# Kernel optimization log

Measured on AMD Instinct MI355X. Metric: run time of the kernel, lower is better.

## Reference

```python
import jax, jax.numpy as jnp
import numpy as np

DIM_MODEL = 512
DIM_HEAD = 64


def setup_inputs() -> dict:
    key = jax.random.key(0)
    ks = jax.random.split(key, 7)
    B, S = 4, 4096
    scale = 1.0 / np.sqrt(DIM_MODEL)
    x = jax.random.normal(ks[0], (B, S, DIM_MODEL), dtype=jnp.float32)
    # nn.Linear weights: stored as [out, in] in torch; we use [in, out] for x @ W
    Wq = jax.random.uniform(ks[1], (DIM_MODEL, DIM_HEAD), jnp.float32, -scale, scale)
    Wk = jax.random.uniform(ks[2], (DIM_MODEL, DIM_HEAD), jnp.float32, -scale, scale)
    Wv = jax.random.uniform(ks[3], (DIM_MODEL, DIM_HEAD), jnp.float32, -scale, scale)
    bq = jax.random.uniform(ks[4], (DIM_HEAD,), jnp.float32, -scale, scale)
    bk = jax.random.uniform(ks[5], (DIM_HEAD,), jnp.float32, -scale, scale)
    bv = jax.random.uniform(ks[6], (DIM_HEAD,), jnp.float32, -scale, scale)
    return {"x": x, "Wq": Wq, "bq": bq, "Wk": Wk, "bk": bk, "Wv": Wv, "bv": bv}


def reference(x, Wq, bq, Wk, bk, Wv, bv):
    # [q,k,v] = z @ U_qkv
    q = x @ Wq + bq  # [B, S, Dh]
    k = x @ Wk + bk
    v = x @ Wv + bv
    dot_scale = jnp.sqrt(jnp.asarray(DIM_HEAD, dtype=x.dtype))
    scores = jnp.einsum("bsd,btd->bst", q, k) / dot_scale  # [B, S, S]
    attn = jax.nn.softmax(scores, axis=-1)
    return jnp.einsum("bst,btd->bsd", attn, v)  # [B, S, Dh]
```

## Files before the change

kernel.cpp:

```cpp
#include <hip/hip_runtime.h>
#include <hip/hip_bf16.h>

typedef short short8 __attribute__((ext_vector_type(8)));
typedef float f32x4 __attribute__((ext_vector_type(4)));

#define MFMA16(a,b,c) __builtin_amdgcn_mfma_f32_16x16x32_bf16((a),(b),(c),0,0,0)

#define NROWS 16384
#define LOG2E 1.44269504088896340736f

#define OFF_Q  0u
#define OFF_K  (2u<<20)
#define OFF_V  (4u<<20)
#define OFF_W  (6u<<20)
#define OFF_O  ((6u<<20) + (1u<<18))

__device__ __forceinline__ unsigned short f2bf(float f){
    union { float f; unsigned u; } v; v.f = f;
    unsigned r = v.u + 0x7FFFu + ((v.u >> 16) & 1u);
    return (unsigned short)(r >> 16);
}
__device__ __forceinline__ unsigned pk2(float a, float b){
    union { __hip_bfloat162 h; unsigned u; } c;
    c.h = __float22bfloat162_rn(make_float2(a, b));
    return c.u;
}

union Frag {
    short8 s;
    unsigned short u[8];
    uint2 d2[2];
    uint4 q4;
};

__global__ __launch_bounds__(256) void wprep_kernel(
    const float* __restrict__ Wq, const float* __restrict__ Wk,
    const float* __restrict__ Wv, unsigned short* __restrict__ wfrag)
{
    int idx = blockIdx.x * 256 + threadIdx.x;
    int lane = idx & 63;
    int rest = idx >> 6;
    int kk = rest & 15;
    int nt = (rest >> 4) & 3;
    int w  = rest >> 6;
    const float* W = (w == 0) ? Wq : (w == 1) ? Wk : Wv;
    float scl = (w == 0) ? (0.125f * LOG2E) : 1.0f;
    int n = 16 * nt + (lane & 15);
    int g = lane >> 4;
    Frag o;
#pragma unroll
    for (int e = 0; e < 8; ++e) {
        int k = 32 * kk + 16 * (e >> 2) + 4 * g + (e & 3);
        o.u[e] = f2bf(W[k * 64 + n] * scl);
    }
    *(uint4*)(wfrag + (size_t)idx * 8) = o.q4;
}

#define LDW(WD, KK) do { \
    _Pragma("unroll") \
    for (int nt_ = 0; nt_ < 4; ++nt_) \
        WD[nt_].q4 = wf[((size_t)(nt_ * 16 + (KK))) * 64 + lane]; \
    } while (0)

#define DOK(WC, KK) do { \
    _Pragma("unroll") \
    for (int M_ = 0; M_ < 2; ++M_) { \
        Frag xf_; \
        const unsigned short* xr_ = &xs[M_ * 16 + l15][32 * (KK) + 4 * g]; \
        xf_.d2[0] = *(const uint2*)xr_; \
        xf_.d2[1] = *(const uint2*)(xr_ + 16); \
        if (w == 2) { \
            _Pragma("unroll") \
            for (int nt_ = 0; nt_ < 4; ++nt_) acc[M_][nt_] = MFMA16(xf_.s, WC[nt_].s, acc[M_][nt_]); \
        } else { \
            _Pragma("unroll") \
            for (int nt_ = 0; nt_ < 4; ++nt_) acc[M_][nt_] = MFMA16(WC[nt_].s, xf_.s, acc[M_][nt_]); \
        } \
    } } while (0)

__global__ __launch_bounds__(192) void qkv_kernel(
    const float* __restrict__ x,
    const float* __restrict__ bq, const float* __restrict__ bk,
    const float* __restrict__ bv,
    const unsigned short* __restrict__ wfrag,
    unsigned short* __restrict__ qfrag,
    unsigned short* __restrict__ kfrag,
    unsigned short* __restrict__ vfrag)
{
    __shared__ unsigned short xs[32][520];
    const int tid = threadIdx.x;
    const int lane = tid & 63;
    const int w = tid >> 6;
    const int l15 = lane & 15, g = lane >> 4;
    const int rg32 = blockIdx.x;
    const float* xbase = x + (size_t)rg32 * 32 * 512;

    for (int i = tid; i < 4096; i += 192) {
        float4 v = *(const float4*)(xbase + i * 4);
        int r_ = i >> 7;
        int c_ = (i & 127) * 4;
        *(uint2*)&xs[r_][c_] = make_uint2(pk2(v.x, v.y), pk2(v.z, v.w));
    }
    __syncthreads();

    f32x4 acc[2][4];
#pragma unroll
    for (int M = 0; M < 2; ++M)
#pragma unroll
        for (int nt = 0; nt < 4; ++nt) acc[M][nt] = (f32x4){0.f,0.f,0.f,0.f};

    const uint4* wf = (const uint4*)wfrag + (size_t)w * 4096;

    Frag wA[4], wB[4];
    LDW(wA, 0);
#pragma unroll
    for (int kp = 0; kp < 8; ++kp) {
        LDW(wB, 2 * kp + 1);
        __builtin_amdgcn_sched_barrier(0);
        DOK(wA, 2 * kp);
        if (2 * kp + 2 < 16) LDW(wA, 2 * kp + 2);
        __builtin_amdgcn_sched_barrier(0);
        DOK(wB, 2 * kp + 1);
    }

#pragma unroll
    for (int M = 0; M < 2; ++M) {
        const int rg  = rg32 * 2 + M;
        const int b   = rg >> 8;
        const int rgb = rg & 255;
        const int tc  = rgb >> 2;
        const int c   = rgb & 3;

        if (w == 0) {
#pragma unroll
            for (int nt = 0; nt < 4; ++nt) {
                float4 bb = *(const float4*)(bq + 16 * nt + 4 * g);
                const float bs = 0.125f * LOG2E;
                float q0 = acc[M][nt][0] + bb.x * bs;
                float q1 = acc[M][nt][1] + bb.y * bs;
                float q2 = acc[M][nt][2] + bb.z * bs;
                float q3 = acc[M][nt][3] + bb.w * bs;
                int ks = nt >> 1, h = nt & 1;
                size_t qoff = ((size_t)(rg * 2 + ks) * 64 + lane) * 8 + h * 4;
                *(uint2*)(qfrag + qoff) = make_uint2(pk2(q0, q1), pk2(q2, q3));
            }
        } else if (w == 1) {
#pragma unroll
            for (int nt = 0; nt < 4; ++nt) {
                float4 bb = *(const float4*)(bk + 16 * nt + 4 * g);
                float k0 = acc[M][nt][0] + bb.x;
                float k1 = acc[M][nt][1] + bb.y;
                float k2 = acc[M][nt][2] + bb.z;
                float k3 = acc[M][nt][3] + bb.w;
                int ks = nt >> 1, h = nt & 1;
                size_t kfi = ((size_t)((b * 64 + tc) * 4 + c) * 2 + ks);
                size_t koff = (kfi * 64 + lane) * 8 + h * 4;
                *(uint2*)(kfrag + koff) = make_uint2(pk2(k0, k1), pk2(k2, k3));
            }
        } else {
            const int vks = c >> 1, vh = c & 1;
#pragma unroll
            for (int nt = 0; nt < 4; ++nt) {
                float bvv = bv[16 * nt + l15];
                float v0 = acc[M][nt][0] + bvv;
                float v1 = acc[M][nt][1] + bvv;
                float v2 = acc[M][nt][2] + bvv;
                float v3 = acc[M][nt][3] + bvv;
                size_t vfi = ((size_t)((b * 64 + tc) * 4 + nt) * 2 + vks);
                size_t voff = (vfi * 64 + lane) * 8 + vh * 4;
                *(uint2*)(vfrag + voff) = make_uint2(pk2(v0, v1), pk2(v2, v3));
            }
        }
    }
}

#define LOADK(KD, CH) do { \
    const uint4* p_ = kb0 + (size_t)(CH) * 512; \
    _Pragma("unroll") \
    for (int c_ = 0; c_ < 4; ++c_) { \
        KD[c_][0].q4 = p_[(c_ * 2 + 0) * 64]; \
        KD[c_][1].q4 = p_[(c_ * 2 + 1) * 64]; \
    } } while (0)

#define LOADV(VD, CH) do { \
    const uint4* p_ = vb0 + (size_t)(CH) * 512; \
    _Pragma("unroll") \
    for (int c_ = 0; c_ < 4; ++c_) { \
        VD[c_][0].q4 = p_[(c_ * 2 + 0) * 64]; \
        VD[c_][1].q4 = p_[(c_ * 2 + 1) * 64]; \
    } } while (0)

#define BODY(KC, KN, CH, CHN) do { \
    Frag vC[4][2]; \
    LOADV(vC, CH); \
    LOADK(KN, CHN); \
    __builtin_amdgcn_sched_barrier(0); \
    _Pragma("unroll") \
    for (int M_ = 0; M_ < 4; ++M_) { \
        f32x4 sD[4]; \
        __builtin_amdgcn_s_setprio(1); \
        _Pragma("unroll") \
        for (int c_ = 0; c_ < 4; ++c_) { \
            f32x4 D = (f32x4){0.f,0.f,0.f,0.f}; \
            D = MFMA16(KC[c_][0].s, qf[M_][0].s, D); \
            D = MFMA16(KC[c_][1].s, qf[M_][1].s, D); \
            sD[c_] = D; \
        } \
        __builtin_amdgcn_s_setprio(0); \
        Frag pa0, pa1; \
        _Pragma("unroll") \
        for (int c_ = 0; c_ < 4; ++c_) { \
            float p0 = __builtin_exp2f(sD[c_][0]); \
            float p1 = __builtin_exp2f(sD[c_][1]); \
            float p2 = __builtin_exp2f(sD[c_][2]); \
            float p3 = __builtin_exp2f(sD[c_][3]); \
            uint2 pk_ = make_uint2(pk2(p0, p1), pk2(p2, p3)); \
            if (c_ < 2) pa0.d2[c_ & 1] = pk_; else pa1.d2[c_ & 1] = pk_; \
        } \
        __builtin_amdgcn_s_setprio(1); \
        lacc[M_] = MFMA16(pa0.s, ones_.s, lacc[M_]); \
        lacc[M_] = MFMA16(pa1.s, ones_.s, lacc[M_]); \
        _Pragma("unroll") \
        for (int dc_ = 0; dc_ < 4; ++dc_) { \
            acc[M_][dc_] = MFMA16(pa0.s, vC[dc_][0].s, acc[M_][dc_]); \
            acc[M_][dc_] = MFMA16(pa1.s, vC[dc_][1].s, acc[M_][dc_]); \
        } \
        __builtin_amdgcn_s_setprio(0); \
    } } while (0)

__global__ __launch_bounds__(256, 2) void attn_kernel(
    const unsigned short* __restrict__ qfrag,
    const unsigned short* __restrict__ kfrag,
    const unsigned short* __restrict__ vfrag,
    uint2* __restrict__ OpartU, float* __restrict__ lml,
    int CPS, int SBITS)
{
    const int tid = threadIdx.x;
    const int lane = tid & 63;
    const int w = tid >> 6;
    const int l15 = lane & 15, g = lane >> 4;
    const int split  = blockIdx.x & ((1 << SBITS) - 1);
    const int qblock = blockIdx.x >> SBITS;
    const int gw = qblock * 4 + w;
    const int b = gw >> 6;
    const int tcg0 = b * 64 + split * CPS;

    const uint4* qf4 = (const uint4*)qfrag;
    const uint4* kb0 = (const uint4*)kfrag + (size_t)tcg0 * 512 + lane;
    const uint4* vb0 = (const uint4*)vfrag + (size_t)tcg0 * 512 + lane;

    Frag qf[4][2];
#pragma unroll
    for (int M = 0; M < 4; ++M)
#pragma unroll
        for (int ks = 0; ks < 2; ++ks)
            qf[M][ks].q4 = qf4[((size_t)((gw * 4 + M) * 2 + ks)) * 64 + lane];

    Frag ones_;
    ones_.d2[0] = make_uint2(0x3F803F80u, 0x3F803F80u);
    ones_.d2[1] = make_uint2(0x3F803F80u, 0x3F803F80u);

    f32x4 acc[4][4], lacc[4];
#pragma unroll
    for (int M = 0; M < 4; ++M) {
        lacc[M] = (f32x4){0.f,0.f,0.f,0.f};
#pragma unroll
        for (int dc = 0; dc < 4; ++dc) acc[M][dc] = (f32x4){0.f,0.f,0.f,0.f};
    }

    Frag kA[4][2], kB[4][2];
    LOADK(kA, 0);

#pragma unroll 1
    for (int ch = 0; ch < CPS; ch += 2) {
        int c1 = (ch + 1 < CPS) ? (ch + 1) : ch;
        int c2 = (ch + 2 < CPS) ? (ch + 2) : ch;
        BODY(kA, kB, ch, c1);
        BODY(kB, kA, c1, c2);
    }

#pragma unroll
    for (int M = 0; M < 4; ++M) {
#pragma unroll
        for (int dc = 0; dc < 4; ++dc)
            OpartU[((size_t)(split * 256 + gw) * 16 + M * 4 + dc) * 64 + lane] =
                make_uint2(pk2(acc[M][dc][0], acc[M][dc][1]),
                           pk2(acc[M][dc][2], acc[M][dc][3]));
        if (l15 == 0)
            *(f32x4*)(lml + (size_t)(split * 256 + gw) * 64 + M * 16 + 4 * g) = lacc[M];
    }
}

__global__ __launch_bounds__(256) void merge_kernel(
    const uint2* __restrict__ OpartU, const float* __restrict__ lml,
    float* __restrict__ out, int S)
{
    int gid = blockIdx.x * 256 + threadIdx.x;
    int lane = gid & 63;
    int dc = (gid >> 6) & 3;
    int M  = (gid >> 8) & 3;
    int gw = gid >> 10;
    int l15 = lane & 15, g = lane >> 4;

    float o0 = 0.f, o1 = 0.f, o2 = 0.f, o3 = 0.f;
    float L0 = 0.f, L1 = 0.f, L2 = 0.f, L3 = 0.f;
    for (int s = 0; s < S; ++s) {
        uint2 pv = OpartU[((size_t)(s * 256 + gw) * 16 + M * 4 + dc) * 64 + lane];
        float4 lv = *(const float4*)(lml + (size_t)(s * 256 + gw) * 64 + M * 16 + 4 * g);
        o0 += __uint_as_float(pv.x << 16);
        o1 += __uint_as_float(pv.x & 0xFFFF0000u);
        o2 += __uint_as_float(pv.y << 16);
        o3 += __uint_as_float(pv.y & 0xFFFF0000u);
        L0 += lv.x; L1 += lv.y; L2 += lv.z; L3 += lv.w;
    }
    size_t row = (size_t)gw * 64 + M * 16 + 4 * g;
    int col = 16 * dc + l15;
    out[(row + 0) * 64 + col] = o0 / L0;
    out[(row + 1) * 64 + col] = o1 / L1;
    out[(row + 2) * 64 + col] = o2 / L2;
    out[(row + 3) * 64 + col] = o3 / L3;
}

extern "C" void kernel_launch(void* const* d_in, const int* in_sizes, int n_in,
                              void* d_out, int out_size, void* d_ws, size_t ws_size,
                              hipStream_t stream) {
    (void)in_sizes; (void)n_in; (void)out_size;
    const float* x  = (const float*)d_in[0];
    const float* Wq = (const float*)d_in[1];
    const float* bq = (const float*)d_in[2];
    const float* Wk = (const float*)d_in[3];
    const float* bk = (const float*)d_in[4];
    const float* Wv = (const float*)d_in[5];
    const float* bv = (const float*)d_in[6];
    float* out = (float*)d_out;

    char* ws = (char*)d_ws;
    unsigned short* qfrag = (unsigned short*)(ws + OFF_Q);
    unsigned short* kfrag = (unsigned short*)(ws + OFF_K);
    unsigned short* vfrag = (unsigned short*)(ws + OFF_V);
    unsigned short* wfrag = (unsigned short*)(ws + OFF_W);

    const size_t oneO = (size_t)256 * 16 * 64 * 8;
    const size_t oneL = (size_t)256 * 64 * 4;
    int S = 8, SBITS = 3;
    if (ws_size < (size_t)OFF_O + 8 * (oneO + oneL)) { S = 4; SBITS = 2; }
    if (ws_size < (size_t)OFF_O + 4 * (oneO + oneL)) { S = 2; SBITS = 1; }
    uint2* OpartU = (uint2*)(ws + OFF_O);
    float* lml    = (float*)(ws + OFF_O + (size_t)S * oneO);
    int CPS = 64 / S;

    hipLaunchKernelGGL(wprep_kernel, dim3(48), dim3(256), 0, stream,
                       Wq, Wk, Wv, wfrag);
    hipLaunchKernelGGL(qkv_kernel, dim3(512), dim3(192), 0, stream,
                       x, bq, bk, bv, wfrag, qfrag, kfrag, vfrag);
    hipLaunchKernelGGL(attn_kernel, dim3(64 * S), dim3(256), 0, stream,
                       qfrag, kfrag, vfrag, OpartU, lml, CPS, SBITS);
    hipLaunchKernelGGL(merge_kernel, dim3(1024), dim3(256), 0, stream,
                       OpartU, lml, out, S);
}
```

Measured before the change: 58.45 us.

## Fuse split-KV merge into attention kernel via last-block atomic counter

Removes the separate merge kernel launch: each attention block increments a per-query-block counter after writing its partial outputs, and the last split to finish reduces all splits and writes the final normalized output. Counters are zeroed in the weight-prep kernel. This saves a launch and its tail, but the merge now runs serially on one block per query block, using fewer threads than the old merge grid and adding threadfence and atomic overhead.

```diff
diff --git a/kernel.cpp b/kernel.cpp
--- a/kernel.cpp
+++ b/kernel.cpp
@@ -35,8 +35,10 @@
 
 __global__ __launch_bounds__(256) void wprep_kernel(
     const float* __restrict__ Wq, const float* __restrict__ Wk,
-    const float* __restrict__ Wv, unsigned short* __restrict__ wfrag)
+    const float* __restrict__ Wv, unsigned short* __restrict__ wfrag,
+    int* __restrict__ cnt)
 {
+    if (blockIdx.x == 0 && threadIdx.x < 256) cnt[threadIdx.x] = 0;
     int idx = blockIdx.x * 256 + threadIdx.x;
     int lane = idx & 63;
     int rest = idx >> 6;
@@ -233,8 +235,10 @@
     const unsigned short* __restrict__ kfrag,
     const unsigned short* __restrict__ vfrag,
     uint2* __restrict__ OpartU, float* __restrict__ lml,
+    int* __restrict__ cnt, float* __restrict__ out,
     int CPS, int SBITS)
 {
+    __shared__ int lastflag;
     const int tid = threadIdx.x;
     const int lane = tid & 63;
     const int w = tid >> 6;
@@ -289,36 +293,42 @@
         if (l15 == 0)
             *(f32x4*)(lml + (size_t)(split * 256 + gw) * 64 + M * 16 + 4 * g) = lacc[M];
     }
-}
-
-__global__ __launch_bounds__(256) void merge_kernel(
-    const uint2* __restrict__ OpartU, const float* __restrict__ lml,
-    float* __restrict__ out, int S)
-{
-    int gid = blockIdx.x * 256 + threadIdx.x;
-    int lane = gid & 63;
-    int dc = (gid >> 6) & 3;
-    int M  = (gid >> 8) & 3;
-    int gw = gid >> 10;
-    int l15 = lane & 15, g = lane >> 4;
-
-    float o0 = 0.f, o1 = 0.f, o2 = 0.f, o3 = 0.f;
-    float L0 = 0.f, L1 = 0.f, L2 = 0.f, L3 = 0.f;
-    for (int s = 0; s < S; ++s) {
-        uint2 pv = OpartU[((size_t)(s * 256 + gw) * 16 + M * 4 + dc) * 64 + lane];
-        float4 lv = *(const float4*)(lml + (size_t)(s * 256 + gw) * 64 + M * 16 + 4 * g);
-        o0 += __uint_as_float(pv.x << 16);
-        o1 += __uint_as_float(pv.x & 0xFFFF0000u);
-        o2 += __uint_as_float(pv.y << 16);
-        o3 += __uint_as_float(pv.y & 0xFFFF0000u);
-        L0 += lv.x; L1 += lv.y; L2 += lv.z; L3 += lv.w;
-    }
-    size_t row = (size_t)gw * 64 + M * 16 + 4 * g;
-    int col = 16 * dc + l15;
-    out[(row + 0) * 64 + col] = o0 / L0;
-    out[(row + 1) * 64 + col] = o1 / L1;
-    out[(row + 2) * 64 + col] = o2 / L2;
-    out[(row + 3) * 64 + col] = o3 / L3;
+
+    __threadfence();
+    if (tid == 0) {
+        int old = atomicAdd(&cnt[qblock], 1);
+        lastflag = (old == (1 << SBITS) - 1);
+    }
+    __syncthreads();
+    if (!lastflag) return;
+    __threadfence();
+
+    const int S = 1 << SBITS;
+    const int dc = (tid >> 6) & 3;
+#pragma unroll 1
+    for (int mw = 0; mw < 4; ++mw) {
+        const int mgw = qblock * 4 + mw;
+#pragma unroll
+        for (int M = 0; M < 4; ++M) {
+            float o0 = 0.f, o1 = 0.f, o2 = 0.f, o3 = 0.f;
+            float L0 = 0.f, L1 = 0.f, L2 = 0.f, L3 = 0.f;
+            for (int s = 0; s < S; ++s) {
+                uint2 pv = OpartU[((size_t)(s * 256 + mgw) * 16 + M * 4 + dc) * 64 + lane];
+                float4 lv = *(const float4*)(lml + (size_t)(s * 256 + mgw) * 64 + M * 16 + 4 * g);
+                o0 += __uint_as_float(pv.x << 16);
+                o1 += __uint_as_float(pv.x & 0xFFFF0000u);
+                o2 += __uint_as_float(pv.y << 16);
+                o3 += __uint_as_float(pv.y & 0xFFFF0000u);
+                L0 += lv.x; L1 += lv.y; L2 += lv.z; L3 += lv.w;
+            }
+            size_t row = (size_t)mgw * 64 + M * 16 + 4 * g;
+            int col = 16 * dc + l15;
+            out[(row + 0) * 64 + col] = o0 / L0;
+            out[(row + 1) * 64 + col] = o1 / L1;
+            out[(row + 2) * 64 + col] = o2 / L2;
+            out[(row + 3) * 64 + col] = o3 / L3;
+        }
+    }
 }
 
 extern "C" void kernel_launch(void* const* d_in, const int* in_sizes, int n_in,
@@ -343,18 +353,17 @@
     const size_t oneO = (size_t)256 * 16 * 64 * 8;
     const size_t oneL = (size_t)256 * 64 * 4;
     int S = 8, SBITS = 3;
-    if (ws_size < (size_t)OFF_O + 8 * (oneO + oneL)) { S = 4; SBITS = 2; }
-    if (ws_size < (size_t)OFF_O + 4 * (oneO + oneL)) { S = 2; SBITS = 1; }
+    if (ws_size < (size_t)OFF_O + 8 * (oneO + oneL) + 1024) { S = 4; SBITS = 2; }
+    if (ws_size < (size_t)OFF_O + 4 * (oneO + oneL) + 1024) { S = 2; SBITS = 1; }
     uint2* OpartU = (uint2*)(ws + OFF_O);
     float* lml    = (float*)(ws + OFF_O + (size_t)S * oneO);
+    int*   cnt    = (int*)(ws + OFF_O + (size_t)S * (oneO + oneL));
     int CPS = 64 / S;
 
     hipLaunchKernelGGL(wprep_kernel, dim3(48), dim3(256), 0, stream,
-                       Wq, Wk, Wv, wfrag);
+                       Wq, Wk, Wv, wfrag, cnt);
     hipLaunchKernelGGL(qkv_kernel, dim3(512), dim3(192), 0, stream,
                        x, bq, bk, bv, wfrag, qfrag, kfrag, vfrag);
     hipLaunchKernelGGL(attn_kernel, dim3(64 * S), dim3(256), 0, stream,
-                       qfrag, kfrag, vfrag, OpartU, lml, CPS, SBITS);
-    hipLaunchKernelGGL(merge_kernel, dim3(1024), dim3(256), 0, stream,
-                       OpartU, lml, out, S);
-}
+                       qfrag, kfrag, vfrag, OpartU, lml, cnt, out, CPS, SBITS);
+}
```

Result: slower. 160.0 us (+173.7%).
